# Optimization experiments

Hardware: AMD Instinct MI355X
Metric: run time of the kernel (lower is better)

Reference implementation:

```python
import jax, jax.numpy as jnp
import numpy as np

EPS = 1e-5

def _bn2d(x, g, b, m, v):
    s = (1, -1, 1, 1)
    return (x - m.reshape(s)) * (g.reshape(s) * jax.lax.rsqrt(v.reshape(s) + EPS)) + b.reshape(s)

def _bn1d(x, g, b, m, v):
    return (x - m) * (g * jax.lax.rsqrt(v + EPS)) + b

def _conv3x3(x, w, b):
    y = jax.lax.conv_general_dilated(x, w, (1, 1), ((1, 1), (1, 1)),
                                     dimension_numbers=('NCHW', 'OIHW', 'NCHW'))
    return y + b.reshape(1, -1, 1, 1)

def setup_inputs() -> dict:
    key = jax.random.key(0)
    ks = iter(jax.random.split(key, 64))
    B = 512
    d = {}
    d['anchor'] = jax.random.normal(next(ks), (B, 1, 16, 8), jnp.float32)
    d['positive'] = jax.random.normal(next(ks), (B, 1, 16, 8), jnp.float32)
    d['negative'] = jax.random.normal(next(ks), (B, 1, 16, 8), jnp.float32)

    def bn_params(c):
        g = jax.random.normal(next(ks), (c,), jnp.float32) * 0.1 + 1.0
        b = jax.random.normal(next(ks), (c,), jnp.float32) * 0.1
        m = jax.random.normal(next(ks), (c,), jnp.float32) * 0.1
        v = jax.random.uniform(next(ks), (c,), jnp.float32, 0.5, 1.5)
        return g, b, m, v

    d['bn0_g'], d['bn0_b'], d['bn0_m'], d['bn0_v'] = bn_params(1)
    d['conv1_w'] = jax.random.normal(next(ks), (64, 1, 3, 3), jnp.float32) * 0.1
    d['conv1_b'] = jax.random.normal(next(ks), (64,), jnp.float32) * 0.1
    d['bn1_g'], d['bn1_b'], d['bn1_m'], d['bn1_v'] = bn_params(64)
    d['conv2_w'] = jax.random.normal(next(ks), (64, 64, 3, 3), jnp.float32) * 0.04
    d['conv2_b'] = jax.random.normal(next(ks), (64,), jnp.float32) * 0.1
    d['bn2_g'], d['bn2_b'], d['bn2_m'], d['bn2_v'] = bn_params(64)
    # locally-connected: kernel_size=1 -> per-position unshared channel mix (o,c,h,w)
    d['lc1_w'] = jax.random.normal(next(ks), (64, 64, 16, 8), jnp.float32) * 0.125
    d['bn3_g'], d['bn3_b'], d['bn3_m'], d['bn3_v'] = bn_params(64)
    d['lc2_w'] = jax.random.normal(next(ks), (64, 64, 16, 8), jnp.float32) * 0.125
    d['bn4_g'], d['bn4_b'], d['bn4_m'], d['bn4_v'] = bn_params(64)
    d['fc1_w'] = jax.random.normal(next(ks), (512, 8192), jnp.float32) * 0.01
    d['fc1_b'] = jax.random.normal(next(ks), (512,), jnp.float32) * 0.1
    d['bnf1_g'], d['bnf1_b'], d['bnf1_m'], d['bnf1_v'] = bn_params(512)
    d['fc2_w'] = jax.random.normal(next(ks), (512, 512), jnp.float32) * 0.04
    d['fc2_b'] = jax.random.normal(next(ks), (512,), jnp.float32) * 0.1
    d['bnf2_g'], d['bnf2_b'], d['bnf2_m'], d['bnf2_v'] = bn_params(512)
    d['fc3_w'] = jax.random.normal(next(ks), (128, 512), jnp.float32) * 0.04
    d['fc3_b'] = jax.random.normal(next(ks), (128,), jnp.float32) * 0.1
    d['bnf3_g'], d['bnf3_b'], d['bnf3_m'], d['bnf3_v'] = bn_params(128)
    d['out_w'] = jax.random.normal(next(ks), (128, 128), jnp.float32) * 0.09
    d['out_b'] = jax.random.normal(next(ks), (128,), jnp.float32) * 0.1
    return d

def _embedding(x, p):
    x = _bn2d(x, p['bn0_g'], p['bn0_b'], p['bn0_m'], p['bn0_v'])
    x = _conv3x3(x, p['conv1_w'], p['conv1_b'])
    x = jax.nn.relu(_bn2d(x, p['bn1_g'], p['bn1_b'], p['bn1_m'], p['bn1_v']))
    x = _conv3x3(x, p['conv2_w'], p['conv2_b'])
    x = jax.nn.relu(_bn2d(x, p['bn2_g'], p['bn2_b'], p['bn2_m'], p['bn2_v']))
    # locally connected (kernel 1): per-position channel mix, no huge unfold intermediate
    x = jnp.einsum('bchw,ochw->bohw', x, p['lc1_w'])
    x = jax.nn.relu(_bn2d(x, p['bn3_g'], p['bn3_b'], p['bn3_m'], p['bn3_v']))
    x = jnp.einsum('bchw,ochw->bohw', x, p['lc2_w'])
    x = jax.nn.relu(_bn2d(x, p['bn4_g'], p['bn4_b'], p['bn4_m'], p['bn4_v']))
    # dropout is identity in eval mode
    x = x.reshape(x.shape[0], -1)  # (B, 8192)
    x = x @ p['fc1_w'].T + p['fc1_b']
    x = jax.nn.relu(_bn1d(x, p['bnf1_g'], p['bnf1_b'], p['bnf1_m'], p['bnf1_v']))
    x = x @ p['fc2_w'].T + p['fc2_b']
    x = jax.nn.relu(_bn1d(x, p['bnf2_g'], p['bnf2_b'], p['bnf2_m'], p['bnf2_v']))
    x = x @ p['fc3_w'].T + p['fc3_b']
    x = jax.nn.relu(_bn1d(x, p['bnf3_g'], p['bnf3_b'], p['bnf3_m'], p['bnf3_v']))
    return x @ p['out_w'].T + p['out_b']

def reference(anchor, positive, negative,
              bn0_g, bn0_b, bn0_m, bn0_v,
              conv1_w, conv1_b, bn1_g, bn1_b, bn1_m, bn1_v,
              conv2_w, conv2_b, bn2_g, bn2_b, bn2_m, bn2_v,
              lc1_w, bn3_g, bn3_b, bn3_m, bn3_v,
              lc2_w, bn4_g, bn4_b, bn4_m, bn4_v,
              fc1_w, fc1_b, bnf1_g, bnf1_b, bnf1_m, bnf1_v,
              fc2_w, fc2_b, bnf2_g, bnf2_b, bnf2_m, bnf2_v,
              fc3_w, fc3_b, bnf3_g, bnf3_b, bnf3_m, bnf3_v,
              out_w, out_b):
    p = dict(bn0_g=bn0_g, bn0_b=bn0_b, bn0_m=bn0_m, bn0_v=bn0_v,
             conv1_w=conv1_w, conv1_b=conv1_b, bn1_g=bn1_g, bn1_b=bn1_b, bn1_m=bn1_m, bn1_v=bn1_v,
             conv2_w=conv2_w, conv2_b=conv2_b, bn2_g=bn2_g, bn2_b=bn2_b, bn2_m=bn2_m, bn2_v=bn2_v,
             lc1_w=lc1_w, bn3_g=bn3_g, bn3_b=bn3_b, bn3_m=bn3_m, bn3_v=bn3_v,
             lc2_w=lc2_w, bn4_g=bn4_g, bn4_b=bn4_b, bn4_m=bn4_m, bn4_v=bn4_v,
             fc1_w=fc1_w, fc1_b=fc1_b, bnf1_g=bnf1_g, bnf1_b=bnf1_b, bnf1_m=bnf1_m, bnf1_v=bnf1_v,
             fc2_w=fc2_w, fc2_b=fc2_b, bnf2_g=bnf2_g, bnf2_b=bnf2_b, bnf2_m=bnf2_m, bnf2_v=bnf2_v,
             fc3_w=fc3_w, fc3_b=fc3_b, bnf3_g=bnf3_g, bnf3_b=bnf3_b, bnf3_m=bnf3_m, bnf3_v=bnf3_v,
             out_w=out_w, out_b=out_b)
    return (_embedding(anchor, p), _embedding(positive, p), _embedding(negative, p))
```

## Files before the change

### kernel.cpp

```cpp
#include <hip/hip_runtime.h>
#include <math.h>

#define EPS 1e-5f
#define FD 8192

typedef __attribute__((ext_vector_type(8))) __bf16 bf16x8;
typedef __attribute__((ext_vector_type(4))) float f32x4;

static __device__ __forceinline__ f32x4 mfma16(bf16x8 a, bf16x8 b, f32x4 c) {
    return __builtin_amdgcn_mfma_f32_16x16x32_bf16(a, b, c, 0, 0, 0);
}

__global__ __launch_bounds__(256) void k_prep_all(
    const float* __restrict__ w1, const float* __restrict__ w2,
    const float* __restrict__ lc1, const float* __restrict__ lc2,
    const float* __restrict__ fc1w, const float* __restrict__ fc2w,
    const float* __restrict__ fc3w, const float* __restrict__ outw,
    __bf16* __restrict__ w1frag, __bf16* __restrict__ w2frag,
    __bf16* __restrict__ lc1frag, __bf16* __restrict__ lc2frag,
    __bf16* __restrict__ fc1Wb, __bf16* __restrict__ wf23) {
    const int bb = blockIdx.x;
    const int t = threadIdx.x;
    __shared__ float wbuf[64][130];

    if (bb == 0) {
        const int lane = t & 63, w = t >> 6;
        const int q = lane >> 4, li = lane & 15;
        const int o = w * 16 + li;
        bf16x8 v;
#pragma unroll
        for (int j = 0; j < 8; ++j) {
            int k = q * 8 + j;
            v[j] = (k < 9) ? (__bf16)w1[o * 9 + k] : (__bf16)0.0f;
        }
        *(bf16x8*)(w1frag + t * 8) = v;
    } else if (bb < 19) {
        const int id = (bb - 1) * 256 + t;
        const int lane = id & 63;
        const int w = (id >> 6) & 3;
        const int chunk = (id >> 8) & 1;
        const int tap = id >> 9;
        const int q = lane >> 4, li = lane & 15;
        const int o = w * 16 + li;
        const int c0 = chunk * 32 + q * 8;
        bf16x8 v;
#pragma unroll
        for (int j = 0; j < 8; ++j)
            v[j] = (__bf16)w2[(o * 64 + c0 + j) * 9 + tap];
        *(bf16x8*)(w2frag + (size_t)id * 8) = v;
    } else if (bb < 147) {
        const int bx = bb - 19;
        const int layer = bx >> 6, o = bx & 63;
        const int wo = o >> 4, lo = o & 15;
        const float* src = (layer ? lc2 : lc1) + (size_t)o * 8192;
        __bf16* dst = layer ? lc2frag : lc1frag;
#pragma unroll
        for (int pass = 0; pass < 8; ++pass) {
            int i = pass * 1024 + t * 4;
            float4 v = *(const float4*)(src + i);
            int c = i >> 7, p = i & 127;
            wbuf[c][p + 0] = v.x; wbuf[c][p + 1] = v.y;
            wbuf[c][p + 2] = v.z; wbuf[c][p + 3] = v.w;
        }
        __syncthreads();
#pragma unroll
        for (int pass = 0; pass < 4; ++pass) {
            int slot = pass * 256 + t;
            int p = slot >> 3, chunk = (slot >> 2) & 1, q = slot & 3;
            bf16x8 v;
#pragma unroll
            for (int j = 0; j < 8; ++j)
                v[j] = (__bf16)wbuf[chunk * 32 + q * 8 + j][p];
            *(bf16x8*)(dst + ((size_t)((p * 2 + chunk) * 4 + wo) * 64 + q * 16 + lo) * 8) = v;
        }
    } else if (bb < 659) {
        const int n = bb - 147;
        const float* src = fc1w + (size_t)n * 8192;
        __bf16* dst = fc1Wb + (size_t)n * 8192;
#pragma unroll
        for (int pass = 0; pass < 8; ++pass) {
            int i = pass * 1024 + t * 4;
            float4 v = *(const float4*)(src + i);
            int c = i >> 7, p = i & 127;
            wbuf[c][p + 0] = v.x; wbuf[c][p + 1] = v.y;
            wbuf[c][p + 2] = v.z; wbuf[c][p + 3] = v.w;
        }
        __syncthreads();
#pragma unroll
        for (int pass = 0; pass < 16; ++pass) {
            int kA = (pass * 256 + t) * 2;
            int c = kA & 63, p = kA >> 6;
            __bf16 tmp[2];
            tmp[0] = (__bf16)wbuf[c][p];
            tmp[1] = (__bf16)wbuf[c + 1][p];
            *(unsigned int*)(dst + kA) = *(unsigned int*)tmp;
        }
    } else {
        int i = (bb - 659) * 256 + t;
        float v;
        if (i < 262144) v = fc2w[i];
        else if (i < 327680) v = fc3w[i - 262144];
        else v = outw[i - 327680];
        wf23[i] = (__bf16)v;
    }
}

__global__ __launch_bounds__(256) void k_conv_mfma(
    const float* __restrict__ inA, const float* __restrict__ inP, const float* __restrict__ inN,
    const float* __restrict__ bn0g, const float* __restrict__ bn0b,
    const float* __restrict__ bn0m, const float* __restrict__ bn0v,
    const __bf16* __restrict__ w1frag, const float* __restrict__ b1,
    const float* __restrict__ bn1g, const float* __restrict__ bn1b,
    const float* __restrict__ bn1m, const float* __restrict__ bn1v,
    const __bf16* __restrict__ w2frag, const float* __restrict__ b2,
    const float* __restrict__ bn2g, const float* __restrict__ bn2b,
    const float* __restrict__ bn2m, const float* __restrict__ bn2v,
    __bf16* __restrict__ act) {
    const int b = blockIdx.x, t = threadIdx.x;
    const int lane = t & 63, w = t >> 6;
    const int q = lane >> 4, li = lane & 15;
    const int n0 = w * 16;
    const float* src = (b < 512 ? inA : (b < 1024 ? inP : inN)) + (size_t)(b & 511) * 128;

    __shared__ __align__(16) float xpad[180];
    __shared__ __align__(16) __bf16 A1[128 * 40];
    __shared__ __align__(16) __bf16 Xp[18 * 12 * 72];
    __shared__ float s1[64], sh1[64], s2[64], sh2[64];

    bf16x8 w1f = *(const bf16x8*)(w1frag + (size_t)(w * 64 + lane) * 8);
    bf16x8 w2f[18];
#pragma unroll
    for (int tap = 0; tap < 9; ++tap)
#pragma unroll
        for (int ch = 0; ch < 2; ++ch)
            w2f[tap * 2 + ch] = *(const bf16x8*)(w2frag +
                ((size_t)((tap * 2 + ch) * 4 + w) * 64 + lane) * 8);

    {
        int* xz = (int*)Xp;
        for (int i = t; i < 7776; i += 256) xz[i] = 0;
        if (t < 180) xpad[t] = 0.f;
        if (t < 64) {
            float sa = bn1g[t] * rsqrtf(bn1v[t] + EPS);
            s1[t] = sa;
            sh1[t] = (b1[t] - bn1m[t]) * sa + bn1b[t];
            float sb = bn2g[t] * rsqrtf(bn2v[t] + EPS);
            s2[t] = sb;
            sh2[t] = (b2[t] - bn2m[t]) * sb + bn2b[t];
        }
    }
    __syncthreads();
    if (t < 128) {
        float s0 = bn0g[0] * rsqrtf(bn0v[0] + EPS);
        float v = (src[t] - bn0m[0]) * s0 + bn0b[0];
        xpad[((t >> 3) + 1) * 10 + (t & 7) + 1] = v;
    }
    __syncthreads();
    {
        int p = t >> 1, half = t & 1;
        int r = p >> 3, cl = p & 7;
        bf16x8 v0, v1;
#pragma unroll
        for (int jj = 0; jj < 8; ++jj) {
            int j = half * 16 + jj;
            v0[jj] = (j < 9) ? (__bf16)xpad[(r + j / 3) * 10 + cl + (j % 3)] : (__bf16)0.f;
            int j2 = half * 16 + 8 + jj;
            v1[jj] = (j2 < 9) ? (__bf16)xpad[(r + j2 / 3) * 10 + cl + (j2 % 3)] : (__bf16)0.f;
        }
        *(bf16x8*)&A1[p * 40 + half * 16] = v0;
        *(bf16x8*)&A1[p * 40 + half * 16 + 8] = v1;
    }
    __syncthreads();
    {
        const float sco = s1[n0 + li], sho = sh1[n0 + li];
        const int o = n0 + li;
#pragma unroll
        for (int m = 0; m < 8; ++m) {
            bf16x8 a = *(const bf16x8*)&A1[(m * 16 + li) * 40 + q * 8];
            f32x4 z = {0.f, 0.f, 0.f, 0.f};
            f32x4 d = mfma16(a, w1f, z);
#pragma unroll
            for (int r = 0; r < 4; ++r) {
                int p = m * 16 + q * 4 + r;
                float v = fmaxf(d[r] * sco + sho, 0.f);
                Xp[(((p >> 3) + 1) * 12 + (p & 7) + 1) * 72 + o] = (__bf16)v;
            }
        }
    }
    __syncthreads();
    f32x4 accA[4], accB[4];
#pragma unroll
    for (int i = 0; i < 4; ++i) {
        accA[i] = (f32x4){0.f, 0.f, 0.f, 0.f};
        accB[i] = (f32x4){0.f, 0.f, 0.f, 0.f};
    }
    {
        const int cl = li & 7;
#pragma unroll
        for (int mp = 0; mp < 4; ++mp) {
            const int r0 = mp * 4 + (li >> 3);
            const int base0 = (r0 * 12 + cl) * 72 + q * 8;
            const int base1 = base0 + 1728;
#pragma unroll
            for (int tap = 0; tap < 9; ++tap) {
                const int tofs = ((tap / 3) * 12 + (tap % 3)) * 72;
#pragma unroll
                for (int ch = 0; ch < 2; ++ch) {
                    bf16x8 a0 = *(const bf16x8*)&Xp[base0 + tofs + ch * 32];
                    bf16x8 a1 = *(const bf16x8*)&Xp[base1 + tofs + ch * 32];
                    accA[mp] = mfma16(a0, w2f[tap * 2 + ch], accA[mp]);
                    accB[mp] = mfma16(a1, w2f[tap * 2 + ch], accB[mp]);
                }
            }
        }
    }
    __syncthreads();
    {
        const float sco = s2[n0 + li], sho = sh2[n0 + li];
        const int o = n0 + li;
#pragma unroll
        for (int mp = 0; mp < 4; ++mp) {
#pragma unroll
            for (int r = 0; r < 4; ++r) {
                int p0 = mp * 32 + q * 4 + r;
                Xp[p0 * 72 + o] = (__bf16)fmaxf(accA[mp][r] * sco + sho, 0.f);
                Xp[(p0 + 16) * 72 + o] = (__bf16)fmaxf(accB[mp][r] * sco + sho, 0.f);
            }
        }
    }
    __syncthreads();
    {
        int p = t >> 1, half = t & 1;
        const __bf16* rp = Xp + p * 72 + half * 32;
        __bf16* ob = act + (size_t)b * FD + p * 64 + half * 32;
        bf16x8 v0 = *(const bf16x8*)rp;
        bf16x8 v1 = *(const bf16x8*)(rp + 8);
        bf16x8 v2 = *(const bf16x8*)(rp + 16);
        bf16x8 v3 = *(const bf16x8*)(rp + 24);
        *(bf16x8*)ob = v0;
        *(bf16x8*)(ob + 8) = v1;
        *(bf16x8*)(ob + 16) = v2;
        *(bf16x8*)(ob + 24) = v3;
    }
}

__global__ __launch_bounds__(256) void k_lc_mfma(
    const __bf16* __restrict__ lc1frag, const __bf16* __restrict__ lc2frag,
    const float* __restrict__ bn3g, const float* __restrict__ bn3b,
    const float* __restrict__ bn3m, const float* __restrict__ bn3v,
    const float* __restrict__ bn4g, const float* __restrict__ bn4b,
    const float* __restrict__ bn4m, const float* __restrict__ bn4v,
    __bf16* __restrict__ act) {
    const int p = blockIdx.x;
    const int b0 = blockIdx.y * 64;
    const int t = threadIdx.x;
    const int lane = t & 63, w = t >> 6;
    const int q = lane >> 4, li = lane & 15;
    const int n0 = w * 16;

    __shared__ __align__(16) __bf16 xs[64 * 72];
    __shared__ __align__(16) __bf16 ys[64 * 72];
    __shared__ float s3[64], sh3[64], s4[64], sh4[64];

    if (t < 64) {
        float sa = bn3g[t] * rsqrtf(bn3v[t] + EPS);
        s3[t] = sa; sh3[t] = bn3b[t] - bn3m[t] * sa;
        float sb = bn4g[t] * rsqrtf(bn4v[t] + EPS);
        s4[t] = sb; sh4[t] = bn4b[t] - bn4m[t] * sb;
    }
    {
        int s = t >> 2, cg = t & 3;
        const __bf16* rp = act + (size_t)(b0 + s) * FD + p * 64 + cg * 16;
        *(bf16x8*)&xs[s * 72 + cg * 16] = *(const bf16x8*)rp;
        *(bf16x8*)&xs[s * 72 + cg * 16 + 8] = *(const bf16x8*)(rp + 8);
    }
    bf16x8 w1a = *(const bf16x8*)(lc1frag + ((size_t)((p * 2 + 0) * 4 + w) * 64 + lane) * 8);
    bf16x8 w1b = *(const bf16x8*)(lc1frag + ((size_t)((p * 2 + 1) * 4 + w) * 64 + lane) * 8);
    bf16x8 w2a = *(const bf16x8*)(lc2frag + ((size_t)((p * 2 + 0) * 4 + w) * 64 + lane) * 8);
    bf16x8 w2b = *(const bf16x8*)(lc2frag + ((size_t)((p * 2 + 1) * 4 + w) * 64 + lane) * 8);
    __syncthreads();
    {
        const float sco = s3[n0 + li], sho = sh3[n0 + li];
#pragma unroll
        for (int m = 0; m < 4; ++m) {
            bf16x8 a0 = *(const bf16x8*)&xs[(m * 16 + li) * 72 + q * 8];
            bf16x8 a1 = *(const bf16x8*)&xs[(m * 16 + li) * 72 + 32 + q * 8];
            f32x4 acc = {0.f, 0.f, 0.f, 0.f};
            acc = mfma16(a0, w1a, acc);
            acc = mfma16(a1, w1b, acc);
#pragma unroll
            for (int r = 0; r < 4; ++r) {
                int bl = m * 16 + q * 4 + r;
                ys[bl * 72 + n0 + li] = (__bf16)fmaxf(acc[r] * sco + sho, 0.f);
            }
        }
    }
    __syncthreads();
    {
        const float sco = s4[n0 + li], sho = sh4[n0 + li];
#pragma unroll
        for (int m = 0; m < 4; ++m) {
            bf16x8 a0 = *(const bf16x8*)&ys[(m * 16 + li) * 72 + q * 8];
            bf16x8 a1 = *(const bf16x8*)&ys[(m * 16 + li) * 72 + 32 + q * 8];
            f32x4 acc = {0.f, 0.f, 0.f, 0.f};
            acc = mfma16(a0, w2a, acc);
            acc = mfma16(a1, w2b, acc);
#pragma unroll
            for (int r = 0; r < 4; ++r) {
                int bl = m * 16 + q * 4 + r;
                xs[bl * 72 + n0 + li] = (__bf16)fmaxf(acc[r] * sco + sho, 0.f);
            }
        }
    }
    __syncthreads();
    {
        int s = t >> 2, cg = t & 3;
        const __bf16* rp = xs + s * 72 + cg * 16;
        __bf16* ob = act + (size_t)(b0 + s) * FD + p * 64 + cg * 16;
        bf16x8 v0 = *(const bf16x8*)rp;
        bf16x8 v1 = *(const bf16x8*)(rp + 8);
        *(bf16x8*)ob = v0;
        *(bf16x8*)(ob + 8) = v1;
    }
}

__global__ __launch_bounds__(256) void k_fc1_mfma(
    const __bf16* __restrict__ A, const __bf16* __restrict__ Wb,
    float* __restrict__ part) {
    const int t = threadIdx.x;
    const int lane = t & 63, w = t >> 6;
    const int q = lane >> 4, li = lane & 15;
    const int m0 = blockIdx.x * 64, n0 = blockIdx.y * 128;
    const int k0 = blockIdx.z * 1024;
    const int wm = (w & 1) * 32, wn = (w >> 1) * 64;

    __shared__ __align__(16) __bf16 As[64 * 40];
    __shared__ __align__(16) __bf16 Bs[128 * 40];

    f32x4 acc[2][4];
#pragma unroll
    for (int i = 0; i < 2; ++i)
#pragma unroll
        for (int j = 0; j < 4; ++j) acc[i][j] = (f32x4){0.f, 0.f, 0.f, 0.f};

    const int rowA = (t & 127) >> 1, rowB = t >> 1, half = t & 1;
    const __bf16* Ag = A + (size_t)(m0 + rowA) * 8192 + k0 + half * 16;
    const __bf16* Bg = Wb + (size_t)(n0 + rowB) * 8192 + k0 + half * 16;

    bf16x8 pa0, pa1, pb0, pb1;
    pb0 = *(const bf16x8*)Bg;
    pb1 = *(const bf16x8*)(Bg + 8);
    if (t < 128) {
        pa0 = *(const bf16x8*)Ag;
        pa1 = *(const bf16x8*)(Ag + 8);
    }

    for (int step = 0; step < 32; ++step) {
        if (t < 128) {
            *(bf16x8*)&As[rowA * 40 + half * 16] = pa0;
            *(bf16x8*)&As[rowA * 40 + half * 16 + 8] = pa1;
        }
        *(bf16x8*)&Bs[rowB * 40 + half * 16] = pb0;
        *(bf16x8*)&Bs[rowB * 40 + half * 16 + 8] = pb1;
        __syncthreads();
        Ag += 32; Bg += 32;
        if (step < 31) {
            pb0 = *(const bf16x8*)Bg;
            pb1 = *(const bf16x8*)(Bg + 8);
            if (t < 128) {
                pa0 = *(const bf16x8*)Ag;
                pa1 = *(const bf16x8*)(Ag + 8);
            }
        }
        bf16x8 af[2], bfr[4];
#pragma unroll
        for (int i = 0; i < 2; ++i)
            af[i] = *(const bf16x8*)&As[(wm + i * 16 + li) * 40 + q * 8];
#pragma unroll
        for (int j = 0; j < 4; ++j)
            bfr[j] = *(const bf16x8*)&Bs[(wn + j * 16 + li) * 40 + q * 8];
#pragma unroll
        for (int i = 0; i < 2; ++i)
#pragma unroll
            for (int j = 0; j < 4; ++j)
                acc[i][j] = mfma16(af[i], bfr[j], acc[i][j]);
        __syncthreads();
    }
    float* pp = part + (size_t)blockIdx.z * 786432;
#pragma unroll
    for (int i = 0; i < 2; ++i) {
#pragma unroll
        for (int r = 0; r < 4; ++r) {
            int m = m0 + wm + i * 16 + q * 4 + r;
#pragma unroll
            for (int j = 0; j < 4; ++j) {
                int n = n0 + wn + j * 16 + li;
                pp[(size_t)m * 512 + n] = acc[i][j][r];
            }
        }
    }
}

__global__ void k_fc1_reduce(const float* __restrict__ part, const float* __restrict__ bias,
                             const float* __restrict__ g, const float* __restrict__ bb,
                             const float* __restrict__ mm, const float* __restrict__ vv,
                             __bf16* __restrict__ out) {
    int gi = blockIdx.x * 256 + threadIdx.x;
    size_t off = (size_t)gi * 4;
    float4 s = make_float4(0.f, 0.f, 0.f, 0.f);
#pragma unroll
    for (int z = 0; z < 8; ++z) {
        float4 v = *(const float4*)(part + (size_t)z * 786432 + off);
        s.x += v.x; s.y += v.y; s.z += v.z; s.w += v.w;
    }
    int n = (gi & 127) * 4;
    float r[4] = {s.x, s.y, s.z, s.w};
    __bf16 o4[4];
#pragma unroll
    for (int j = 0; j < 4; ++j) {
        float sc = g[n + j] * rsqrtf(vv[n + j] + EPS);
        float x = (r[j] + bias[n + j] - mm[n + j]) * sc + bb[n + j];
        o4[j] = (__bf16)fmaxf(x, 0.f);
    }
    *(uint2*)(out + off) = *(uint2*)o4;
}

__global__ __launch_bounds__(256) void k_fc2_mfma(
    const __bf16* __restrict__ A, const __bf16* __restrict__ W,
    const float* __restrict__ bias,
    const float* __restrict__ bng, const float* __restrict__ bnb,
    const float* __restrict__ bnm, const float* __restrict__ bnv,
    __bf16* __restrict__ out) {
    const int t = threadIdx.x;
    const int lane = t & 63, w = t >> 6;
    const int q = lane >> 4, li = lane & 15;
    const int m0 = blockIdx.x * 64, n0 = blockIdx.y * 64;
    const int wm = (w & 1) * 32, wn = (w >> 1) * 32;
    const int K = 512, N = 512;

    __shared__ __align__(16) __bf16 As[64 * 40];
    __shared__ __align__(16) __bf16 Bs[64 * 40];

    f32x4 acc[2][2];
#pragma unroll
    for (int i = 0; i < 2; ++i)
#pragma unroll
        for (int j = 0; j < 2; ++j) acc[i][j] = (f32x4){0.f, 0.f, 0.f, 0.f};

    const int row = (t & 127) >> 1, half = t & 1;
    const __bf16* g = (t < 128 ? A + (size_t)(m0 + row) * K
                               : W + (size_t)(n0 + row) * K) + half * 16;
    __bf16* ld = (t < 128 ? As : Bs) + row * 40 + half * 16;

    bf16x8 p0 = *(const bf16x8*)g;
    bf16x8 p1 = *(const bf16x8*)(g + 8);
    for (int k0 = 0; k0 < K; k0 += 32) {
        *(bf16x8*)ld = p0;
        *(bf16x8*)(ld + 8) = p1;
        __syncthreads();
        g += 32;
        if (k0 + 32 < K) {
            p0 = *(const bf16x8*)g;
            p1 = *(const bf16x8*)(g + 8);
        }
        bf16x8 af[2], bfr[2];
#pragma unroll
        for (int i = 0; i < 2; ++i)
            af[i] = *(const bf16x8*)&As[(wm + i * 16 + li) * 40 + q * 8];
#pragma unroll
        for (int j = 0; j < 2; ++j)
            bfr[j] = *(const bf16x8*)&Bs[(wn + j * 16 + li) * 40 + q * 8];
#pragma unroll
        for (int i = 0; i < 2; ++i)
#pragma unroll
            for (int j = 0; j < 2; ++j)
                acc[i][j] = mfma16(af[i], bfr[j], acc[i][j]);
        __syncthreads();
    }
    float bi[2], sc[2], hh[2];
#pragma unroll
    for (int j = 0; j < 2; ++j) {
        int n = n0 + wn + j * 16 + li;
        bi[j] = bias[n];
        sc[j] = bng[n] * rsqrtf(bnv[n] + EPS);
        hh[j] = bnb[n] - bnm[n] * sc[j];
    }
#pragma unroll
    for (int i = 0; i < 2; ++i) {
#pragma unroll
        for (int r = 0; r < 4; ++r) {
            int m = m0 + wm + i * 16 + q * 4 + r;
#pragma unroll
            for (int j = 0; j < 2; ++j) {
                int n = n0 + wn + j * 16 + li;
                float x = (acc[i][j][r] + bi[j]) * sc[j] + hh[j];
                out[(size_t)m * N + n] = (__bf16)fmaxf(x, 0.f);
            }
        }
    }
}

__global__ __launch_bounds__(256) void k_fc3out(
    const __bf16* __restrict__ A, const __bf16* __restrict__ W3,
    const __bf16* __restrict__ Wo,
    const float* __restrict__ b3,
    const float* __restrict__ bng, const float* __restrict__ bnb,
    const float* __restrict__ bnm, const float* __restrict__ bnv,
    const float* __restrict__ bo, float* __restrict__ out) {
    const int t = threadIdx.x;
    const int lane = t & 63, w = t >> 6;
    const int q = lane >> 4, li = lane & 15;
    const int m0 = blockIdx.x * 64;
    const int wn = w * 32;

    __shared__ __align__(16) __bf16 As[64 * 40];
    __shared__ __align__(16) __bf16 Bs[128 * 40];
    __shared__ __align__(16) __bf16 ysb[64 * 136];

    const int rowA = (t & 127) >> 1, rowB = t >> 1, half = t & 1;
    const __bf16* Ag = A + (size_t)(m0 + rowA) * 512 + half * 16;
    const __bf16* Bg = W3 + (size_t)rowB * 512 + half * 16;

    f32x4 acc[4][2];
#pragma unroll
    for (int i = 0; i < 4; ++i)
#pragma unroll
        for (int j = 0; j < 2; ++j) acc[i][j] = (f32x4){0.f, 0.f, 0.f, 0.f};

    bf16x8 pa0, pa1, pb0, pb1;
    pb0 = *(const bf16x8*)Bg;
    pb1 = *(const bf16x8*)(Bg + 8);
    if (t < 128) {
        pa0 = *(const bf16x8*)Ag;
        pa1 = *(const bf16x8*)(Ag + 8);
    }
    for (int step = 0; step < 16; ++step) {
        if (t < 128) {
            *(bf16x8*)&As[rowA * 40 + half * 16] = pa0;
            *(bf16x8*)&As[rowA * 40 + half * 16 + 8] = pa1;
        }
        *(bf16x8*)&Bs[rowB * 40 + half * 16] = pb0;
        *(bf16x8*)&Bs[rowB * 40 + half * 16 + 8] = pb1;
        __syncthreads();
        Ag += 32; Bg += 32;
        if (step < 15) {
            pb0 = *(const bf16x8*)Bg;
            pb1 = *(const bf16x8*)(Bg + 8);
            if (t < 128) {
                pa0 = *(const bf16x8*)Ag;
                pa1 = *(const bf16x8*)(Ag + 8);
            }
        }
        bf16x8 af[4], bfr[2];
#pragma unroll
        for (int i = 0; i < 4; ++i)
            af[i] = *(const bf16x8*)&As[(i * 16 + li) * 40 + q * 8];
#pragma unroll
        for (int j = 0; j < 2; ++j)
            bfr[j] = *(const bf16x8*)&Bs[(wn + j * 16 + li) * 40 + q * 8];
#pragma unroll
        for (int i = 0; i < 4; ++i)
#pragma unroll
            for (int j = 0; j < 2; ++j)
                acc[i][j] = mfma16(af[i], bfr[j], acc[i][j]);
        __syncthreads();
    }
    {
#pragma unroll
        for (int j = 0; j < 2; ++j) {
            int n = wn + j * 16 + li;
            float sc = bng[n] * rsqrtf(bnv[n] + EPS);
            float hh = bnb[n] - bnm[n] * sc;
            float bi = b3[n];
#pragma unroll
            for (int i = 0; i < 4; ++i)
#pragma unroll
                for (int r = 0; r < 4; ++r) {
                    int ml = i * 16 + q * 4 + r;
                    float x = (acc[i][j][r] + bi) * sc + hh;
                    ysb[ml * 136 + n] = (__bf16)fmaxf(x, 0.f);
                }
        }
    }
    __syncthreads();
    f32x4 acc2[4][2];
#pragma unroll
    for (int i = 0; i < 4; ++i)
#pragma unroll
        for (int j = 0; j < 2; ++j) acc2[i][j] = (f32x4){0.f, 0.f, 0.f, 0.f};
    const __bf16* Bg2 = Wo + (size_t)rowB * 128 + half * 16;
#pragma unroll
    for (int step = 0; step < 4; ++step) {
        *(bf16x8*)&Bs[rowB * 40 + half * 16] = *(const bf16x8*)(Bg2 + step * 32);
        *(bf16x8*)&Bs[rowB * 40 + half * 16 + 8] = *(const bf16x8*)(Bg2 + step * 32 + 8);
        __syncthreads();
        bf16x8 af[4], bfr[2];
#pragma unroll
        for (int i = 0; i < 4; ++i)
            af[i] = *(const bf16x8*)&ysb[(i * 16 + li) * 136 + step * 32 + q * 8];
#pragma unroll
        for (int j = 0; j < 2; ++j)
            bfr[j] = *(const bf16x8*)&Bs[(wn + j * 16 + li) * 40 + q * 8];
#pragma unroll
        for (int i = 0; i < 4; ++i)
#pragma unroll
            for (int j = 0; j < 2; ++j)
                acc2[i][j] = mfma16(af[i], bfr[j], acc2[i][j]);
        __syncthreads();
    }
#pragma unroll
    for (int j = 0; j < 2; ++j) {
        int n = wn + j * 16 + li;
        float bi = bo[n];
#pragma unroll
        for (int i = 0; i < 4; ++i)
#pragma unroll
            for (int r = 0; r < 4; ++r) {
                int m = m0 + i * 16 + q * 4 + r;
                out[(size_t)m * 128 + n] = acc2[i][j][r] + bi;
            }
    }
}

extern "C" void kernel_launch(void* const* d_in, const int* in_sizes, int n_in,
                              void* d_out, int out_size, void* d_ws, size_t ws_size,
                              hipStream_t stream) {
    const float* inA    = (const float*)d_in[0];
    const float* inP    = (const float*)d_in[1];
    const float* inN    = (const float*)d_in[2];
    const float* bn0g   = (const float*)d_in[3];
    const float* bn0b   = (const float*)d_in[4];
    const float* bn0m   = (const float*)d_in[5];
    const float* bn0v   = (const float*)d_in[6];
    const float* conv1w = (const float*)d_in[7];
    const float* conv1b = (const float*)d_in[8];
    const float* bn1g   = (const float*)d_in[9];
    const float* bn1b   = (const float*)d_in[10];
    const float* bn1m   = (const float*)d_in[11];
    const float* bn1v   = (const float*)d_in[12];
    const float* conv2w = (const float*)d_in[13];
    const float* conv2b = (const float*)d_in[14];
    const float* bn2g   = (const float*)d_in[15];
    const float* bn2b   = (const float*)d_in[16];
    const float* bn2m   = (const float*)d_in[17];
    const float* bn2v   = (const float*)d_in[18];
    const float* lc1w   = (const float*)d_in[19];
    const float* bn3g   = (const float*)d_in[20];
    const float* bn3b   = (const float*)d_in[21];
    const float* bn3m   = (const float*)d_in[22];
    const float* bn3v   = (const float*)d_in[23];
    const float* lc2w   = (const float*)d_in[24];
    const float* bn4g   = (const float*)d_in[25];
    const float* bn4b   = (const float*)d_in[26];
    const float* bn4m   = (const float*)d_in[27];
    const float* bn4v   = (const float*)d_in[28];
    const float* fc1w   = (const float*)d_in[29];
    const float* fc1b   = (const float*)d_in[30];
    const float* bnf1g  = (const float*)d_in[31];
    const float* bnf1b  = (const float*)d_in[32];
    const float* bnf1m  = (const float*)d_in[33];
    const float* bnf1v  = (const float*)d_in[34];
    const float* fc2w   = (const float*)d_in[35];
    const float* fc2b   = (const float*)d_in[36];
    const float* bnf2g  = (const float*)d_in[37];
    const float* bnf2b  = (const float*)d_in[38];
    const float* bnf2m  = (const float*)d_in[39];
    const float* bnf2v  = (const float*)d_in[40];
    const float* fc3w   = (const float*)d_in[41];
    const float* fc3b   = (const float*)d_in[42];
    const float* bnf3g  = (const float*)d_in[43];
    const float* bnf3b  = (const float*)d_in[44];
    const float* bnf3m  = (const float*)d_in[45];
    const float* bnf3v  = (const float*)d_in[46];
    const float* outw   = (const float*)d_in[47];
    const float* outb   = (const float*)d_in[48];

    char* wsb = (char*)d_ws;
    __bf16* w1frag  = (__bf16*)wsb;
    __bf16* w2frag  = w1frag + 2048;
    __bf16* lc1frag = w2frag + 36864;
    __bf16* lc2frag = lc1frag + 524288;
    __bf16* fc1Wb   = lc2frag + 524288;
    __bf16* wf23    = fc1Wb + 4194304;
    __bf16* act     = wf23 + 344064;
    __bf16* act3    = act + 12582912;
    __bf16* act4    = act3 + 786432;
    float*  part    = (float*)(((uintptr_t)(act4 + 786432) + 15) & ~(uintptr_t)15);
    __bf16* wf2 = wf23;
    __bf16* wf3 = wf23 + 262144;
    __bf16* wfo = wf23 + 327680;

    k_prep_all<<<2003, 256, 0, stream>>>(conv1w, conv2w, lc1w, lc2w,
        fc1w, fc2w, fc3w, outw, w1frag, w2frag, lc1frag, lc2frag, fc1Wb, wf23);

    k_conv_mfma<<<1536, 256, 0, stream>>>(inA, inP, inN,
        bn0g, bn0b, bn0m, bn0v, w1frag, conv1b, bn1g, bn1b, bn1m, bn1v,
        w2frag, conv2b, bn2g, bn2b, bn2m, bn2v, act);

    k_lc_mfma<<<dim3(128, 24), 256, 0, stream>>>(lc1frag, lc2frag,
        bn3g, bn3b, bn3m, bn3v, bn4g, bn4b, bn4m, bn4v, act);

    k_fc1_mfma<<<dim3(24, 4, 8), 256, 0, stream>>>(act, fc1Wb, part);
    k_fc1_reduce<<<768, 256, 0, stream>>>(part, fc1b, bnf1g, bnf1b, bnf1m, bnf1v, act3);

    k_fc2_mfma<<<dim3(24, 8), 256, 0, stream>>>(act3, wf2, fc2b,
        bnf2g, bnf2b, bnf2m, bnf2v, act4);

    k_fc3out<<<24, 256, 0, stream>>>(act4, wf3, wfo, fc3b,
        bnf3g, bnf3b, bnf3m, bnf3v, outb, (float*)d_out);
}
```

Before: 250.8 us.

## Overlap weight conversion with conv kernel and retile LC and FC1 GEMMs

```diff
diff --git a/kernel.cpp b/kernel.cpp
--- a/kernel.cpp
+++ b/kernel.cpp
@@ -11,18 +11,10 @@
     return __builtin_amdgcn_mfma_f32_16x16x32_bf16(a, b, c, 0, 0, 0);
 }
 
-__global__ __launch_bounds__(256) void k_prep_all(
+__global__ __launch_bounds__(256) void k_prep_frags(
     const float* __restrict__ w1, const float* __restrict__ w2,
-    const float* __restrict__ lc1, const float* __restrict__ lc2,
-    const float* __restrict__ fc1w, const float* __restrict__ fc2w,
-    const float* __restrict__ fc3w, const float* __restrict__ outw,
-    __bf16* __restrict__ w1frag, __bf16* __restrict__ w2frag,
-    __bf16* __restrict__ lc1frag, __bf16* __restrict__ lc2frag,
-    __bf16* __restrict__ fc1Wb, __bf16* __restrict__ wf23) {
-    const int bb = blockIdx.x;
-    const int t = threadIdx.x;
-    __shared__ float wbuf[64][130];
-
+    __bf16* __restrict__ w1frag, __bf16* __restrict__ w2frag) {
+    const int bb = blockIdx.x, t = threadIdx.x;
     if (bb == 0) {
         const int lane = t & 63, w = t >> 6;
         const int q = lane >> 4, li = lane & 15;
@@ -34,7 +26,7 @@
             v[j] = (k < 9) ? (__bf16)w1[o * 9 + k] : (__bf16)0.0f;
         }
         *(bf16x8*)(w1frag + t * 8) = v;
-    } else if (bb < 19) {
+    } else {
         const int id = (bb - 1) * 256 + t;
         const int lane = id & 63;
         const int w = (id >> 6) & 3;
@@ -48,64 +40,10 @@
         for (int j = 0; j < 8; ++j)
             v[j] = (__bf16)w2[(o * 64 + c0 + j) * 9 + tap];
         *(bf16x8*)(w2frag + (size_t)id * 8) = v;
-    } else if (bb < 147) {
-        const int bx = bb - 19;
-        const int layer = bx >> 6, o = bx & 63;
-        const int wo = o >> 4, lo = o & 15;
-        const float* src = (layer ? lc2 : lc1) + (size_t)o * 8192;
-        __bf16* dst = layer ? lc2frag : lc1frag;
-#pragma unroll
-        for (int pass = 0; pass < 8; ++pass) {
-            int i = pass * 1024 + t * 4;
-            float4 v = *(const float4*)(src + i);
-            int c = i >> 7, p = i & 127;
-            wbuf[c][p + 0] = v.x; wbuf[c][p + 1] = v.y;
-            wbuf[c][p + 2] = v.z; wbuf[c][p + 3] = v.w;
-        }
-        __syncthreads();
-#pragma unroll
-        for (int pass = 0; pass < 4; ++pass) {
-            int slot = pass * 256 + t;
-            int p = slot >> 3, chunk = (slot >> 2) & 1, q = slot & 3;
-            bf16x8 v;
-#pragma unroll
-            for (int j = 0; j < 8; ++j)
-                v[j] = (__bf16)wbuf[chunk * 32 + q * 8 + j][p];
-            *(bf16x8*)(dst + ((size_t)((p * 2 + chunk) * 4 + wo) * 64 + q * 16 + lo) * 8) = v;
-        }
-    } else if (bb < 659) {
-        const int n = bb - 147;
-        const float* src = fc1w + (size_t)n * 8192;
-        __bf16* dst = fc1Wb + (size_t)n * 8192;
-#pragma unroll
-        for (int pass = 0; pass < 8; ++pass) {
-            int i = pass * 1024 + t * 4;
-            float4 v = *(const float4*)(src + i);
-            int c = i >> 7, p = i & 127;
-            wbuf[c][p + 0] = v.x; wbuf[c][p + 1] = v.y;
-            wbuf[c][p + 2] = v.z; wbuf[c][p + 3] = v.w;
-        }
-        __syncthreads();
-#pragma unroll
-        for (int pass = 0; pass < 16; ++pass) {
-            int kA = (pass * 256 + t) * 2;
-            int c = kA & 63, p = kA >> 6;
-            __bf16 tmp[2];
-            tmp[0] = (__bf16)wbuf[c][p];
-            tmp[1] = (__bf16)wbuf[c + 1][p];
-            *(unsigned int*)(dst + kA) = *(unsigned int*)tmp;
-        }
-    } else {
-        int i = (bb - 659) * 256 + t;
-        float v;
-        if (i < 262144) v = fc2w[i];
-        else if (i < 327680) v = fc3w[i - 262144];
-        else v = outw[i - 327680];
-        wf23[i] = (__bf16)v;
-    }
-}
-
-__global__ __launch_bounds__(256) void k_conv_mfma(
+    }
+}
+
+__global__ __launch_bounds__(256) void k_conv_mega(
     const float* __restrict__ inA, const float* __restrict__ inP, const float* __restrict__ inN,
     const float* __restrict__ bn0g, const float* __restrict__ bn0b,
     const float* __restrict__ bn0m, const float* __restrict__ bn0v,
@@ -115,17 +53,89 @@
     const __bf16* __restrict__ w2frag, const float* __restrict__ b2,
     const float* __restrict__ bn2g, const float* __restrict__ bn2b,
     const float* __restrict__ bn2m, const float* __restrict__ bn2v,
-    __bf16* __restrict__ act) {
-    const int b = blockIdx.x, t = threadIdx.x;
+    __bf16* __restrict__ act,
+    const float* __restrict__ lc1, const float* __restrict__ lc2,
+    const float* __restrict__ fc1w, const float* __restrict__ fc2w,
+    const float* __restrict__ fc3w, const float* __restrict__ outw,
+    __bf16* __restrict__ lc1frag, __bf16* __restrict__ lc2frag,
+    __bf16* __restrict__ fc1Wb, __bf16* __restrict__ wf23) {
+    const int bb = blockIdx.x;
+    const int t = threadIdx.x;
+    __shared__ __align__(16) char smem[43136];
+
+    if (bb >= 1536) {
+        const int pb = bb - 1536;
+        float (*wbuf)[130] = (float(*)[130])smem;
+        if (pb < 128) {
+            const int layer = pb >> 6, o = pb & 63;
+            const int wo = o >> 4, lo = o & 15;
+            const float* src = (layer ? lc2 : lc1) + (size_t)o * 8192;
+            __bf16* dst = layer ? lc2frag : lc1frag;
+#pragma unroll
+            for (int pass = 0; pass < 8; ++pass) {
+                int i = pass * 1024 + t * 4;
+                float4 v = *(const float4*)(src + i);
+                int c = i >> 7, p = i & 127;
+                wbuf[c][p + 0] = v.x; wbuf[c][p + 1] = v.y;
+                wbuf[c][p + 2] = v.z; wbuf[c][p + 3] = v.w;
+            }
+            __syncthreads();
+#pragma unroll
+            for (int pass = 0; pass < 4; ++pass) {
+                int slot = pass * 256 + t;
+                int p = slot >> 3, chunk = (slot >> 2) & 1, q = slot & 3;
+                bf16x8 v;
+#pragma unroll
+                for (int j = 0; j < 8; ++j)
+                    v[j] = (__bf16)wbuf[chunk * 32 + q * 8 + j][p];
+                *(bf16x8*)(dst + ((size_t)((p * 2 + chunk) * 4 + wo) * 64 + q * 16 + lo) * 8) = v;
+            }
+        } else if (pb < 640) {
+            const int n = pb - 128;
+            const float* src = fc1w + (size_t)n * 8192;
+            __bf16* dst = fc1Wb + (size_t)n * 8192;
+#pragma unroll
+            for (int pass = 0; pass < 8; ++pass) {
+                int i = pass * 1024 + t * 4;
+                float4 v = *(const float4*)(src + i);
+                int c = i >> 7, p = i & 127;
+                wbuf[c][p + 0] = v.x; wbuf[c][p + 1] = v.y;
+                wbuf[c][p + 2] = v.z; wbuf[c][p + 3] = v.w;
+            }
+            __syncthreads();
+#pragma unroll
+            for (int pass = 0; pass < 16; ++pass) {
+                int kA = (pass * 256 + t) * 2;
+                int c = kA & 63, p = kA >> 6;
+                __bf16 tmp[2];
+                tmp[0] = (__bf16)wbuf[c][p];
+                tmp[1] = (__bf16)wbuf[c + 1][p];
+                *(unsigned int*)(dst + kA) = *(unsigned int*)tmp;
+            }
+        } else {
+            int i = (pb - 640) * 256 + t;
+            float v;
+            if (i < 262144) v = fc2w[i];
+            else if (i < 327680) v = fc3w[i - 262144];
+            else v = outw[i - 327680];
+            wf23[i] = (__bf16)v;
+        }
+        return;
+    }
+
+    const int b = bb;
     const int lane = t & 63, w = t >> 6;
     const int q = lane >> 4, li = lane & 15;
     const int n0 = w * 16;
     const float* src = (b < 512 ? inA : (b < 1024 ? inP : inN)) + (size_t)(b & 511) * 128;
 
-    __shared__ __align__(16) float xpad[180];
-    __shared__ __align__(16) __bf16 A1[128 * 40];
-    __shared__ __align__(16) __bf16 Xp[18 * 12 * 72];
-    __shared__ float s1[64], sh1[64], s2[64], sh2[64];
+    float* xpad = (float*)smem;
+    __bf16* A1 = (__bf16*)(smem + 768);
+    __bf16* Xp = (__bf16*)(smem + 11008);
+    float* s1 = (float*)(smem + 42112);
+    float* sh1 = (float*)(smem + 42368);
+    float* s2 = (float*)(smem + 42624);
+    float* sh2 = (float*)(smem + 42880);
 
     bf16x8 w1f = *(const bf16x8*)(w1frag + (size_t)(w * 64 + lane) * 8);
     bf16x8 w2f[18];
@@ -252,14 +262,14 @@
     const float* __restrict__ bn4m, const float* __restrict__ bn4v,
     __bf16* __restrict__ act) {
     const int p = blockIdx.x;
-    const int b0 = blockIdx.y * 64;
+    const int b0 = blockIdx.y * 128;
     const int t = threadIdx.x;
     const int lane = t & 63, w = t >> 6;
     const int q = lane >> 4, li = lane & 15;
     const int n0 = w * 16;
 
-    __shared__ __align__(16) __bf16 xs[64 * 72];
-    __shared__ __align__(16) __bf16 ys[64 * 72];
+    __shared__ __align__(16) __bf16 xs[128 * 72];
+    __shared__ __align__(16) __bf16 ys[128 * 72];
     __shared__ float s3[64], sh3[64], s4[64], sh4[64];
 
     if (t < 64) {
@@ -269,10 +279,13 @@
         s4[t] = sb; sh4[t] = bn4b[t] - bn4m[t] * sb;
     }
     {
-        int s = t >> 2, cg = t & 3;
-        const __bf16* rp = act + (size_t)(b0 + s) * FD + p * 64 + cg * 16;
-        *(bf16x8*)&xs[s * 72 + cg * 16] = *(const bf16x8*)rp;
-        *(bf16x8*)&xs[s * 72 + cg * 16 + 8] = *(const bf16x8*)(rp + 8);
+        int s = t >> 1, half = t & 1;
+        const __bf16* rp = act + (size_t)(b0 + s) * FD + p * 64 + half * 32;
+        __bf16* xp = xs + s * 72 + half * 32;
+        *(bf16x8*)xp = *(const bf16x8*)rp;
+        *(bf16x8*)(xp + 8) = *(const bf16x8*)(rp + 8);
+        *(bf16x8*)(xp + 16) = *(const bf16x8*)(rp + 16);
+        *(bf16x8*)(xp + 24) = *(const bf16x8*)(rp + 24);
     }
     bf16x8 w1a = *(const bf16x8*)(lc1frag + ((size_t)((p * 2 + 0) * 4 + w) * 64 + lane) * 8);
     bf16x8 w1b = *(const bf16x8*)(lc1frag + ((size_t)((p * 2 + 1) * 4 + w) * 64 + lane) * 8);
@@ -282,7 +295,7 @@
     {
         const float sco = s3[n0 + li], sho = sh3[n0 + li];
 #pragma unroll
-        for (int m = 0; m < 4; ++m) {
+        for (int m = 0; m < 8; ++m) {
             bf16x8 a0 = *(const bf16x8*)&xs[(m * 16 + li) * 72 + q * 8];
             bf16x8 a1 = *(const bf16x8*)&xs[(m * 16 + li) * 72 + 32 + q * 8];
             f32x4 acc = {0.f, 0.f, 0.f, 0.f};
@@ -299,7 +312,7 @@
     {
         const float sco = s4[n0 + li], sho = sh4[n0 + li];
 #pragma unroll
-        for (int m = 0; m < 4; ++m) {
+        for (int m = 0; m < 8; ++m) {
             bf16x8 a0 = *(const bf16x8*)&ys[(m * 16 + li) * 72 + q * 8];
             bf16x8 a1 = *(const bf16x8*)&ys[(m * 16 + li) * 72 + 32 + q * 8];
             f32x4 acc = {0.f, 0.f, 0.f, 0.f};
@@ -314,13 +327,17 @@
     }
     __syncthreads();
     {
-        int s = t >> 2, cg = t & 3;
-        const __bf16* rp = xs + s * 72 + cg * 16;
-        __bf16* ob = act + (size_t)(b0 + s) * FD + p * 64 + cg * 16;
+        int s = t >> 1, half = t & 1;
+        const __bf16* rp = xs + s * 72 + half * 32;
+        __bf16* ob = act + (size_t)(b0 + s) * FD + p * 64 + half * 32;
         bf16x8 v0 = *(const bf16x8*)rp;
         bf16x8 v1 = *(const bf16x8*)(rp + 8);
+        bf16x8 v2 = *(const bf16x8*)(rp + 16);
+        bf16x8 v3 = *(const bf16x8*)(rp + 24);
         *(bf16x8*)ob = v0;
         *(bf16x8*)(ob + 8) = v1;
+        *(bf16x8*)(ob + 16) = v2;
+        *(bf16x8*)(ob + 24) = v3;
     }
 }
 
@@ -330,60 +347,56 @@
     const int t = threadIdx.x;
     const int lane = t & 63, w = t >> 6;
     const int q = lane >> 4, li = lane & 15;
-    const int m0 = blockIdx.x * 64, n0 = blockIdx.y * 128;
-    const int k0 = blockIdx.z * 1024;
-    const int wm = (w & 1) * 32, wn = (w >> 1) * 64;
-
-    __shared__ __align__(16) __bf16 As[64 * 40];
-    __shared__ __align__(16) __bf16 Bs[128 * 40];
-
-    f32x4 acc[2][4];
+    const int m0 = blockIdx.x * 64, n0 = blockIdx.y * 64;
+    const int k0 = blockIdx.z * 2048;
+    const int wm = (w & 1) * 32, wn = (w >> 1) * 32;
+
+    __shared__ __align__(16) __bf16 As[64 * 72];
+    __shared__ __align__(16) __bf16 Bs[64 * 72];
+
+    f32x4 acc[2][2];
 #pragma unroll
     for (int i = 0; i < 2; ++i)
 #pragma unroll
-        for (int j = 0; j < 4; ++j) acc[i][j] = (f32x4){0.f, 0.f, 0.f, 0.f};
-
-    const int rowA = (t & 127) >> 1, rowB = t >> 1, half = t & 1;
-    const __bf16* Ag = A + (size_t)(m0 + rowA) * 8192 + k0 + half * 16;
-    const __bf16* Bg = Wb + (size_t)(n0 + rowB) * 8192 + k0 + half * 16;
-
-    bf16x8 pa0, pa1, pb0, pb1;
-    pb0 = *(const bf16x8*)Bg;
-    pb1 = *(const bf16x8*)(Bg + 8);
-    if (t < 128) {
-        pa0 = *(const bf16x8*)Ag;
-        pa1 = *(const bf16x8*)(Ag + 8);
-    }
+        for (int j = 0; j < 2; ++j) acc[i][j] = (f32x4){0.f, 0.f, 0.f, 0.f};
+
+    const int row = t >> 2, qt = t & 3;
+    const __bf16* Ag = A + (size_t)(m0 + row) * 8192 + k0 + qt * 16;
+    const __bf16* Bg = Wb + (size_t)(n0 + row) * 8192 + k0 + qt * 16;
+
+    bf16x8 pa0 = *(const bf16x8*)Ag;
+    bf16x8 pa1 = *(const bf16x8*)(Ag + 8);
+    bf16x8 pb0 = *(const bf16x8*)Bg;
+    bf16x8 pb1 = *(const bf16x8*)(Bg + 8);
 
     for (int step = 0; step < 32; ++step) {
-        if (t < 128) {
-            *(bf16x8*)&As[rowA * 40 + half * 16] = pa0;
-            *(bf16x8*)&As[rowA * 40 + half * 16 + 8] = pa1;
-        }
-        *(bf16x8*)&Bs[rowB * 40 + half * 16] = pb0;
-        *(bf16x8*)&Bs[rowB * 40 + half * 16 + 8] = pb1;
+        *(bf16x8*)&As[row * 72 + qt * 16] = pa0;
+        *(bf16x8*)&As[row * 72 + qt * 16 + 8] = pa1;
+        *(bf16x8*)&Bs[row * 72 + qt * 16] = pb0;
+        *(bf16x8*)&Bs[row * 72 + qt * 16 + 8] = pb1;
         __syncthreads();
-        Ag += 32; Bg += 32;
+        Ag += 64; Bg += 64;
         if (step < 31) {
+            pa0 = *(const bf16x8*)Ag;
+            pa1 = *(const bf16x8*)(Ag + 8);
             pb0 = *(const bf16x8*)Bg;
             pb1 = *(const bf16x8*)(Bg + 8);
-            if (t < 128) {
-                pa0 = *(const bf16x8*)Ag;
-                pa1 = *(const bf16x8*)(Ag + 8);
-            }
-        }
-        bf16x8 af[2], bfr[4];
-#pragma unroll
-        for (int i = 0; i < 2; ++i)
-            af[i] = *(const bf16x8*)&As[(wm + i * 16 + li) * 40 + q * 8];
-#pragma unroll
-        for (int j = 0; j < 4; ++j)
-            bfr[j] = *(const bf16x8*)&Bs[(wn + j * 16 + li) * 40 + q * 8];
-#pragma unroll
-        for (int i = 0; i < 2; ++i)
-#pragma unroll
-            for (int j = 0; j < 4; ++j)
-                acc[i][j] = mfma16(af[i], bfr[j], acc[i][j]);
+        }
+#pragma unroll
+        for (int kc = 0; kc < 2; ++kc) {
+            bf16x8 af[2], bfr[2];
+#pragma unroll
+            for (int i = 0; i < 2; ++i)
+                af[i] = *(const bf16x8*)&As[(wm + i * 16 + li) * 72 + kc * 32 + q * 8];
+#pragma unroll
+            for (int j = 0; j < 2; ++j)
+                bfr[j] = *(const bf16x8*)&Bs[(wn + j * 16 + li) * 72 + kc * 32 + q * 8];
+#pragma unroll
+            for (int i = 0; i < 2; ++i)
+#pragma unroll
+                for (int j = 0; j < 2; ++j)
+                    acc[i][j] = mfma16(af[i], bfr[j], acc[i][j]);
+        }
         __syncthreads();
     }
     float* pp = part + (size_t)blockIdx.z * 786432;
@@ -393,7 +406,7 @@
         for (int r = 0; r < 4; ++r) {
             int m = m0 + wm + i * 16 + q * 4 + r;
 #pragma unroll
-            for (int j = 0; j < 4; ++j) {
+            for (int j = 0; j < 2; ++j) {
                 int n = n0 + wn + j * 16 + li;
                 pp[(size_t)m * 512 + n] = acc[i][j][r];
             }
@@ -409,7 +422,7 @@
     size_t off = (size_t)gi * 4;
     float4 s = make_float4(0.f, 0.f, 0.f, 0.f);
 #pragma unroll
-    for (int z = 0; z < 8; ++z) {
+    for (int z = 0; z < 4; ++z) {
         float4 v = *(const float4*)(part + (size_t)z * 786432 + off);
         s.x += v.x; s.y += v.y; s.z += v.z; s.w += v.w;
     }
@@ -690,17 +703,18 @@
     __bf16* wf3 = wf23 + 262144;
     __bf16* wfo = wf23 + 327680;
 
-    k_prep_all<<<2003, 256, 0, stream>>>(conv1w, conv2w, lc1w, lc2w,
-        fc1w, fc2w, fc3w, outw, w1frag, w2frag, lc1frag, lc2frag, fc1Wb, wf23);
-
-    k_conv_mfma<<<1536, 256, 0, stream>>>(inA, inP, inN,
+    k_prep_frags<<<19, 256, 0, stream>>>(conv1w, conv2w, w1frag, w2frag);
+
+    k_conv_mega<<<3520, 256, 0, stream>>>(inA, inP, inN,
         bn0g, bn0b, bn0m, bn0v, w1frag, conv1b, bn1g, bn1b, bn1m, bn1v,
-        w2frag, conv2b, bn2g, bn2b, bn2m, bn2v, act);
-
-    k_lc_mfma<<<dim3(128, 24), 256, 0, stream>>>(lc1frag, lc2frag,
+        w2frag, conv2b, bn2g, bn2b, bn2m, bn2v, act,
+        lc1w, lc2w, fc1w, fc2w, fc3w, outw,
+        lc1frag, lc2frag, fc1Wb, wf23);
+
+    k_lc_mfma<<<dim3(128, 12), 256, 0, stream>>>(lc1frag, lc2frag,
         bn3g, bn3b, bn3m, bn3v, bn4g, bn4b, bn4m, bn4v, act);
 
-    k_fc1_mfma<<<dim3(24, 4, 8), 256, 0, stream>>>(act, fc1Wb, part);
+    k_fc1_mfma<<<dim3(24, 8, 4), 256, 0, stream>>>(act, fc1Wb, part);
     k_fc1_reduce<<<768, 256, 0, stream>>>(part, fc1b, bnf1g, bnf1b, bnf1m, bnf1v, act3);
 
     k_fc2_mfma<<<dim3(24, 8), 256, 0, stream>>>(act3, wf2, fc2b,
```

After: 252.9 us. Within noise of the previous version (+0.8%).
